# Kernel optimization log

Hardware: AMD Instinct MI355X
Metric: run time of the kernel (lower is better)

Reference implementation:

```python
import jax, jax.numpy as jnp
import numpy as np

N_NODES = 50000
N_EDGES = 600000
IN_DIM = 128
LATENT = 128
OUT_DIM = 40
NUM_LAYERS = 2


def setup_inputs() -> dict:
    key = jax.random.key(0)
    ks = jax.random.split(key, 8)
    nodes_feats = jax.random.normal(ks[0], (N_NODES, IN_DIM), dtype=jnp.float32)
    adj_list = jax.random.randint(ks[1], (N_EDGES, 2), 0, N_NODES, dtype=jnp.int64)
    s_in = 1.0 / np.sqrt(IN_DIM)
    s_cb = 1.0 / np.sqrt(2 * LATENT)
    s_out = 1.0 / np.sqrt(LATENT)
    W_in = jax.random.uniform(ks[2], (IN_DIM, LATENT), jnp.float32, -s_in, s_in)
    b_in = jnp.zeros((LATENT,), jnp.float32)
    W_comb = jax.random.uniform(ks[3], (NUM_LAYERS, 2 * LATENT, LATENT), jnp.float32, -s_cb, s_cb)
    b_comb = jnp.zeros((NUM_LAYERS, LATENT), jnp.float32)
    W_out = jax.random.uniform(ks[4], (LATENT, OUT_DIM), jnp.float32, -s_out, s_out)
    b_out = jnp.zeros((OUT_DIM,), jnp.float32)
    return {"nodes_feats": nodes_feats, "adj_list": adj_list, "W_in": W_in, "b_in": b_in,
            "W_comb": W_comb, "b_comb": b_comb, "W_out": W_out, "b_out": b_out}


def reference(nodes_feats, adj_list, W_in, b_in, W_comb, b_comb, W_out, b_out):
    n = nodes_feats.shape[0]
    fro = adj_list[:, 0]
    to = adj_list[:, 1]
    # initialize: project input features to latent space
    h = jax.nn.relu(nodes_feats @ W_in + b_in)  # [N, LATENT]
    # in-degree for mean aggregation (replaces per-node Python stack+mean)
    deg = jax.ops.segment_sum(jnp.ones(fro.shape[0], h.dtype), to, num_segments=n)
    inv_deg = 1.0 / jnp.maximum(deg, 1.0)  # guard isolated nodes
    for l in range(W_comb.shape[0]):
        # gather neighbor feats along edges, scatter-add to destinations, mean
        msg = jax.ops.segment_sum(h[fro], to, num_segments=n) * inv_deg[:, None]
        # combine: ReLU(Linear([node || message]))
        h = jax.nn.relu(jnp.concatenate([h, msg], axis=-1) @ W_comb[l] + b_comb[l])
    # output head (logits for CrossEntropyLoss)
    return h @ W_out + b_out
```

## Files before the change

kernel.cpp:

```cpp
#include <hip/hip_runtime.h>
#include <hip/hip_fp16.h>

#define N_NODES 50000
#define N_EDGES 600000
#define NBLK 49

typedef unsigned int u32;
typedef _Float16 v8h __attribute__((ext_vector_type(8)));
typedef _Float16 v4h __attribute__((ext_vector_type(4)));
typedef float v4f __attribute__((ext_vector_type(4)));

__device__ __forceinline__ float2 h2f2(u32 u) {
    __half2 h = *(__half2*)&u;
    return __half22float2(h);
}

__device__ __forceinline__ int calc_mode(const int* __restrict__ adj_w) {
    int l = threadIdx.x & 63;
    unsigned long long b = __ballot(adj_w[2 * l + 1] != 0);
    return (b == 0ull) ? 1 : 0;
}
__device__ __forceinline__ int adj_to(const int* a, int m, int e) {
    return m ? a[4 * e + 2] : a[2 * e + 1];
}
__device__ __forceinline__ int adj_fro(const int* a, int m, int e) {
    return m ? a[4 * e] : a[2 * e];
}

#define CNT_B   293
#define WPREP_B 344
#define IN_B    1563

__global__ void k_count_prep(const int* __restrict__ adj_w, int* __restrict__ deg,
                             int* __restrict__ rank,
                             const float* __restrict__ W_in,
                             const float* __restrict__ W_comb,
                             const float* __restrict__ W_out,
                             _Float16* __restrict__ WinT,
                             _Float16* __restrict__ WcombT,
                             _Float16* __restrict__ WoutT) {
    if (blockIdx.x < CNT_B) {
        int m = calc_mode(adj_w);
        int base = blockIdx.x * 2048 + threadIdx.x;
        int to[8], r[8];
#pragma unroll
        for (int i = 0; i < 8; i++) {
            int e = base + i * 256;
            to[i] = (e < N_EDGES) ? adj_to(adj_w, m, e) : -1;
        }
#pragma unroll
        for (int i = 0; i < 8; i++)
            if (to[i] >= 0) r[i] = atomicAdd(&deg[to[i]], 1);
#pragma unroll
        for (int i = 0; i < 8; i++) {
            int e = base + i * 256;
            if (e < N_EDGES) rank[e] = r[i];
        }
        return;
    }
    int idx = (blockIdx.x - CNT_B) * 256 + threadIdx.x;
    if (idx < 16384) {
        int n = idx & 127, k = idx >> 7;
        WinT[n * 128 + k] = (_Float16)W_in[k * 128 + n];
    } else if (idx < 16384 + 65536) {
        int j = idx - 16384;
        int l = j >> 15, r = j & 32767;
        int n = r & 127, k = r >> 7;
        WcombT[l * 32768 + n * 256 + k] = (_Float16)W_comb[l * 32768 + k * 128 + n];
    } else if (idx < 16384 + 65536 + 6144) {
        int j = idx - 81920;
        int n = j >> 7, k = j & 127;
        WoutT[n * 128 + k] = (n < 40) ? (_Float16)W_out[k * 40 + n] : (_Float16)0.f;
    }
}

__global__ void k_scan1(const int* __restrict__ deg, int* __restrict__ row_ptr,
                        int* __restrict__ bsum) {
    __shared__ int s[1024];
    int tid = threadIdx.x, i = blockIdx.x * 1024 + tid;
    int v = (i < N_NODES) ? deg[i] : 0;
    s[tid] = v;
    __syncthreads();
    for (int off = 1; off < 1024; off <<= 1) {
        int t = (tid >= off) ? s[tid - off] : 0;
        __syncthreads();
        s[tid] += t;
        __syncthreads();
    }
    if (i < N_NODES) row_ptr[i] = s[tid] - v;
    if (tid == 1023) bsum[blockIdx.x] = s[1023];
}

__global__ void k_scan23(const int* __restrict__ deg, int* __restrict__ row_ptr,
                         const int* __restrict__ bsum, float* __restrict__ inv_deg) {
    __shared__ int sbase;
    int tid = threadIdx.x;
    if (tid < 64) {
        int v = (tid < NBLK && tid < (int)blockIdx.x) ? bsum[tid] : 0;
#pragma unroll
        for (int off = 32; off > 0; off >>= 1) v += __shfl_down(v, off);
        if (tid == 0) sbase = v;
    }
    __syncthreads();
    int i = blockIdx.x * 1024 + tid;
    if (i < N_NODES) {
        row_ptr[i] = row_ptr[i] + sbase;
        inv_deg[i] = 1.0f / fmaxf((float)deg[i], 1.0f);
    }
    if (i == 0) row_ptr[N_NODES] = N_EDGES;
}

__global__ __launch_bounds__(256, 2) void k_fill_in(const int* __restrict__ adj_w,
                                                    const int* __restrict__ row_ptr,
                                                    const int* __restrict__ rank,
                                                    int* __restrict__ edge_src,
                                                    const float* __restrict__ X,
                                                    const _Float16* __restrict__ WT,
                                                    const float* __restrict__ bias,
                                                    _Float16* __restrict__ h) {
    __shared__ __align__(16) _Float16 xs[32][136];
    if (blockIdx.x < CNT_B) {
        int m = calc_mode(adj_w);
        int base = blockIdx.x * 2048 + threadIdx.x;
        int to[8], fro[8], rk[8];
#pragma unroll
        for (int i = 0; i < 8; i++) {
            int e = base + i * 256;
            if (e < N_EDGES) {
                to[i] = adj_to(adj_w, m, e);
                fro[i] = adj_fro(adj_w, m, e);
                rk[i] = rank[e];
            } else {
                to[i] = -1;
            }
        }
#pragma unroll
        for (int i = 0; i < 8; i++)
            if (to[i] >= 0) edge_src[row_ptr[to[i]] + rk[i]] = fro[i];
        return;
    }
    const int t0 = threadIdx.x, w = t0 >> 6, l = t0 & 63;
    const int R0 = (blockIdx.x - CNT_B) * 32;
    const float4* X4 = (const float4*)X;
#pragma unroll
    for (int i = 0; i < 4; i++) {
        int idx = i * 256 + t0;
        int row = idx >> 5, c4 = idx & 31;
        int rr = R0 + row;
        if (rr > N_NODES - 1) rr = N_NODES - 1;
        float4 v = X4[(size_t)rr * 32 + c4];
        v4h hv = {(_Float16)v.x, (_Float16)v.y, (_Float16)v.z, (_Float16)v.w};
        *(v4h*)&xs[row][c4 * 4] = hv;
    }
    const int ch = w & 1, rh = w >> 1;
    v8h wf[4][4];
#pragma unroll
    for (int t = 0; t < 4; t++)
#pragma unroll
        for (int s = 0; s < 4; s++) {
            int n = ch * 64 + t * 16 + (l & 15);
            int k = s * 32 + (l >> 4) * 8;
            wf[t][s] = *(const v8h*)&WT[n * 128 + k];
        }
    v4f acc[4];
#pragma unroll
    for (int t = 0; t < 4; t++) acc[t] = (v4f){0.f, 0.f, 0.f, 0.f};
    __syncthreads();
#pragma unroll
    for (int s = 0; s < 4; s++) {
        v8h a = *(const v8h*)&xs[rh * 16 + (l & 15)][s * 32 + (l >> 4) * 8];
#pragma unroll
        for (int t = 0; t < 4; t++)
            acc[t] = __builtin_amdgcn_mfma_f32_16x16x32_f16(a, wf[t][s], acc[t], 0, 0, 0);
    }
#pragma unroll
    for (int t = 0; t < 4; t++) {
        int col = ch * 64 + t * 16 + (l & 15);
        float b = bias[col];
#pragma unroll
        for (int i = 0; i < 4; i++) {
            int row = R0 + rh * 16 + (l >> 4) * 4 + i;
            if (row < N_NODES)
                h[(size_t)row * 128 + col] = (_Float16)fmaxf(acc[t][i] + b, 0.f);
        }
    }
}

__global__ __launch_bounds__(256) void k_gather(const uint2* __restrict__ h4,
                                                uint2* __restrict__ msg4,
                                                const int* __restrict__ row_ptr,
                                                const int* __restrict__ edge_src,
                                                const float* __restrict__ inv_deg) {
    const int w = threadIdx.x >> 6, l = threadIdx.x & 63;
    const int half = l >> 5, c = l & 31;
    const int wid = blockIdx.x * 4 + w, nw = gridDim.x * 4;
    for (int row = wid; row < N_NODES; row += nw) {
        const int e0 = row_ptr[row], e1 = row_ptr[row + 1];
        float a0 = 0.f, a1 = 0.f, a2 = 0.f, a3 = 0.f;
        for (int bse = e0; bse < e1; bse += 8) {
            uint2 v[4];
#pragma unroll
            for (int i = 0; i < 4; i++) {
                int ee = bse + 2 * i + half;
                int idx = (ee < e1) ? ee : (e1 - 1);
                v[i] = h4[(size_t)edge_src[idx] * 32 + c];
            }
#pragma unroll
            for (int i = 0; i < 4; i++) {
                if (bse + 2 * i + half < e1) {
                    float2 f0 = h2f2(v[i].x), f1 = h2f2(v[i].y);
                    a0 += f0.x;
                    a1 += f0.y;
                    a2 += f1.x;
                    a3 += f1.y;
                }
            }
        }
        a0 += __shfl_xor(a0, 32);
        a1 += __shfl_xor(a1, 32);
        a2 += __shfl_xor(a2, 32);
        a3 += __shfl_xor(a3, 32);
        if (half == 0) {
            const float inv = inv_deg[row];
            __half2 o0 = __floats2half2_rn(a0 * inv, a1 * inv);
            __half2 o1 = __floats2half2_rn(a2 * inv, a3 * inv);
            uint2 o;
            o.x = *(u32*)&o0;
            o.y = *(u32*)&o1;
            msg4[(size_t)row * 32 + c] = o;
        }
    }
}

__global__ __launch_bounds__(256, 2) void k_layer(const _Float16* __restrict__ hin,
                                                  const _Float16* __restrict__ msg,
                                                  const _Float16* __restrict__ WT,
                                                  const float* __restrict__ bias,
                                                  _Float16* __restrict__ hout) {
    __shared__ __align__(16) _Float16 xs[64][264];
    const int t0 = threadIdx.x, w = t0 >> 6, l = t0 & 63;
    const int R0 = blockIdx.x * 64;
    const uint4* h4 = (const uint4*)hin;
    const uint4* m4 = (const uint4*)msg;
#pragma unroll
    for (int i = 0; i < 8; i++) {
        int idx = i * 256 + t0;
        int row = idx >> 5, c16 = idx & 31;
        int rr = R0 + row;
        if (rr > N_NODES - 1) rr = N_NODES - 1;
        uint4 v = (c16 < 16) ? h4[(size_t)rr * 16 + c16] : m4[(size_t)rr * 16 + (c16 - 16)];
        *(uint4*)&xs[row][c16 * 8] = v;
    }
    const int ch = w & 1, rh = w >> 1;
    v8h wf[4][8];
#pragma unroll
    for (int t = 0; t < 4; t++)
#pragma unroll
        for (int s = 0; s < 8; s++) {
            int n = ch * 64 + t * 16 + (l & 15);
            int k = s * 32 + (l >> 4) * 8;
            wf[t][s] = *(const v8h*)&WT[n * 256 + k];
        }
    v4f acc[2][4];
#pragma unroll
    for (int sub = 0; sub < 2; sub++)
#pragma unroll
        for (int t = 0; t < 4; t++) acc[sub][t] = (v4f){0.f, 0.f, 0.f, 0.f};
    __syncthreads();
#pragma unroll
    for (int s = 0; s < 8; s++) {
#pragma unroll
        for (int sub = 0; sub < 2; sub++) {
            v8h a = *(const v8h*)&xs[rh * 32 + sub * 16 + (l & 15)][s * 32 + (l >> 4) * 8];
#pragma unroll
            for (int t = 0; t < 4; t++)
                acc[sub][t] = __builtin_amdgcn_mfma_f32_16x16x32_f16(a, wf[t][s], acc[sub][t], 0, 0, 0);
        }
    }
#pragma unroll
    for (int sub = 0; sub < 2; sub++)
#pragma unroll
        for (int t = 0; t < 4; t++) {
            int col = ch * 64 + t * 16 + (l & 15);
            float b = bias[col];
#pragma unroll
            for (int i = 0; i < 4; i++) {
                int row = R0 + rh * 32 + sub * 16 + (l >> 4) * 4 + i;
                if (row < N_NODES)
                    hout[(size_t)row * 128 + col] = (_Float16)fmaxf(acc[sub][t][i] + b, 0.f);
            }
        }
}

__global__ __launch_bounds__(256, 2) void k_layer_out(const _Float16* __restrict__ hin,
                                                      const _Float16* __restrict__ msg,
                                                      const _Float16* __restrict__ WT,
                                                      const float* __restrict__ bias,
                                                      const _Float16* __restrict__ WoT,
                                                      const float* __restrict__ bias_o,
                                                      float* __restrict__ outp) {
    __shared__ __align__(16) _Float16 xs[64][264];
    const int t0 = threadIdx.x, w = t0 >> 6, l = t0 & 63;
    const int R0 = blockIdx.x * 64;
    const uint4* h4 = (const uint4*)hin;
    const uint4* m4 = (const uint4*)msg;
#pragma unroll
    for (int i = 0; i < 8; i++) {
        int idx = i * 256 + t0;
        int row = idx >> 5, c16 = idx & 31;
        int rr = R0 + row;
        if (rr > N_NODES - 1) rr = N_NODES - 1;
        uint4 v = (c16 < 16) ? h4[(size_t)rr * 16 + c16] : m4[(size_t)rr * 16 + (c16 - 16)];
        *(uint4*)&xs[row][c16 * 8] = v;
    }
    const int ch = w & 1, rh = w >> 1;
    v8h wf[4][8];
#pragma unroll
    for (int t = 0; t < 4; t++)
#pragma unroll
        for (int s = 0; s < 8; s++) {
            int n = ch * 64 + t * 16 + (l & 15);
            int k = s * 32 + (l >> 4) * 8;
            wf[t][s] = *(const v8h*)&WT[n * 256 + k];
        }
    v4f acc[2][4];
#pragma unroll
    for (int sub = 0; sub < 2; sub++)
#pragma unroll
        for (int t = 0; t < 4; t++) acc[sub][t] = (v4f){0.f, 0.f, 0.f, 0.f};
    __syncthreads();
#pragma unroll
    for (int s = 0; s < 8; s++) {
#pragma unroll
        for (int sub = 0; sub < 2; sub++) {
            v8h a = *(const v8h*)&xs[rh * 32 + sub * 16 + (l & 15)][s * 32 + (l >> 4) * 8];
#pragma unroll
            for (int t = 0; t < 4; t++)
                acc[sub][t] = __builtin_amdgcn_mfma_f32_16x16x32_f16(a, wf[t][s], acc[sub][t], 0, 0, 0);
        }
    }
    __syncthreads();
    _Float16* hs = &xs[0][0];
#pragma unroll
    for (int sub = 0; sub < 2; sub++)
#pragma unroll
        for (int t = 0; t < 4; t++) {
            int col = ch * 64 + t * 16 + (l & 15);
            float b = bias[col];
#pragma unroll
            for (int i = 0; i < 4; i++) {
                int lrow = rh * 32 + sub * 16 + (l >> 4) * 4 + i;
                hs[lrow * 136 + col] = (_Float16)fmaxf(acc[sub][t][i] + b, 0.f);
            }
        }
    v8h wo[3][4];
#pragma unroll
    for (int t = 0; t < 3; t++)
#pragma unroll
        for (int s = 0; s < 4; s++) {
            int n = t * 16 + (l & 15);
            int k = s * 32 + (l >> 4) * 8;
            wo[t][s] = *(const v8h*)&WoT[n * 128 + k];
        }
    v4f acc2[3];
#pragma unroll
    for (int t = 0; t < 3; t++) acc2[t] = (v4f){0.f, 0.f, 0.f, 0.f};
    __syncthreads();
#pragma unroll
    for (int s = 0; s < 4; s++) {
        v8h a = *(const v8h*)&hs[(w * 16 + (l & 15)) * 136 + s * 32 + (l >> 4) * 8];
#pragma unroll
        for (int t = 0; t < 3; t++)
            acc2[t] = __builtin_amdgcn_mfma_f32_16x16x32_f16(a, wo[t][s], acc2[t], 0, 0, 0);
    }
#pragma unroll
    for (int t = 0; t < 3; t++) {
        int col = t * 16 + (l & 15);
        if (col < 40) {
            float b = bias_o[col];
#pragma unroll
            for (int i = 0; i < 4; i++) {
                int row = R0 + w * 16 + (l >> 4) * 4 + i;
                if (row < N_NODES) outp[(size_t)row * 40 + col] = acc2[t][i] + b;
            }
        }
    }
}

extern "C" void kernel_launch(void* const* d_in, const int* in_sizes, int n_in,
                              void* d_out, int out_size, void* d_ws, size_t ws_size,
                              hipStream_t stream) {
    int ix[8] = {0, 1, 2, 3, 4, 5, 6, 7};
    int tmp[8] = {-1, -1, -1, -1, -1, -1, -1, -1};
    for (int i = 0; i < n_in && i < 8; i++) {
        switch (in_sizes[i]) {
            case 6400000: tmp[0] = i; break;
            case 1200000: case 2400000: tmp[1] = i; break;
            case 16384:   tmp[2] = i; break;
            case 128:     tmp[3] = i; break;
            case 65536:   tmp[4] = i; break;
            case 256:     tmp[5] = i; break;
            case 5120:    tmp[6] = i; break;
            case 40:      tmp[7] = i; break;
        }
    }
    int found = 0;
    for (int j = 0; j < 8; j++) found += (tmp[j] >= 0);
    if (found == 8) for (int j = 0; j < 8; j++) ix[j] = tmp[j];

    const float* X      = (const float*)d_in[ix[0]];
    const int*   adj_w  = (const int*)d_in[ix[1]];
    const float* W_in   = (const float*)d_in[ix[2]];
    const float* b_in   = (const float*)d_in[ix[3]];
    const float* W_comb = (const float*)d_in[ix[4]];
    const float* b_comb = (const float*)d_in[ix[5]];
    const float* W_out  = (const float*)d_in[ix[6]];
    const float* b_out  = (const float*)d_in[ix[7]];
    float* out = (float*)d_out;

    char* base = (char*)d_ws;
    int*      deg      = (int*)(base + 0);
    int*      row_ptr  = (int*)(base + 200000);
    int*      rank     = (int*)(base + 400004);
    float*    inv_deg  = (float*)(base + 2800004);
    int*      edge_src = (int*)(base + 3000008);
    _Float16* WinT     = (_Float16*)(base + 5400016);
    _Float16* WcombT   = (_Float16*)(base + 5432784);
    _Float16* WoutT    = (_Float16*)(base + 5563856);
    _Float16* hA       = (_Float16*)(base + 5576144);
    _Float16* hB       = (_Float16*)(base + 18376144);
    _Float16* msg      = (_Float16*)(base + 31176144);
    int*      bsum     = (int*)hA;

    hipMemsetAsync(deg, 0, N_NODES * sizeof(int), stream);
    k_count_prep<<<CNT_B + WPREP_B, 256, 0, stream>>>(adj_w, deg, rank, W_in, W_comb, W_out,
                                                      WinT, WcombT, WoutT);
    k_scan1<<<NBLK, 1024, 0, stream>>>(deg, row_ptr, bsum);
    k_scan23<<<NBLK, 1024, 0, stream>>>(deg, row_ptr, bsum, inv_deg);
    k_fill_in<<<CNT_B + IN_B, 256, 0, stream>>>(adj_w, row_ptr, rank, edge_src,
                                                X, WinT, b_in, hA);

    k_gather<<<2048, 256, 0, stream>>>((const uint2*)hA, (uint2*)msg, row_ptr, edge_src, inv_deg);
    k_layer<<<782, 256, 0, stream>>>(hA, msg, WcombT, b_comb, hB);

    k_gather<<<2048, 256, 0, stream>>>((const uint2*)hB, (uint2*)msg, row_ptr, edge_src, inv_deg);
    k_layer_out<<<782, 256, 0, stream>>>(hB, msg, WcombT + 32768, b_comb + 128,
                                         WoutT, b_out, out);
}
```

Measured before the change: 254.8 us.

## Widen gather loads, fuse scan kernels via decoupled lookback, vectorize edge loads

The gather kernel now uses 16-byte loads, with four 16-lane groups each handling one edge and one row's 128 halves. It also prefetches the next row's row_ptr bounds. The two scan kernels are merged into one that passes block sums through flag-tagged atomics in the workspace, which removes one launch and the row_ptr re-read. Edge-list reads become single vector loads of (fro,to), and the memset now also clears the sync flags. The single-pass scan assumes all 49 blocks are co-resident, which holds on this GPU but adds spin-wait risk.

```diff
diff --git a/kernel.cpp b/kernel.cpp
--- a/kernel.cpp
+++ b/kernel.cpp
@@ -20,11 +20,17 @@
     unsigned long long b = __ballot(adj_w[2 * l + 1] != 0);
     return (b == 0ull) ? 1 : 0;
 }
-__device__ __forceinline__ int adj_to(const int* a, int m, int e) {
-    return m ? a[4 * e + 2] : a[2 * e + 1];
-}
-__device__ __forceinline__ int adj_fro(const int* a, int m, int e) {
-    return m ? a[4 * e] : a[2 * e];
+__device__ __forceinline__ void load_edge(const int* __restrict__ a, int m, int e,
+                                          int& fro, int& to) {
+    if (m) {
+        uint4 v = ((const uint4*)a)[e];
+        fro = (int)v.x;
+        to = (int)v.z;
+    } else {
+        uint2 v = ((const uint2*)a)[e];
+        fro = (int)v.x;
+        to = (int)v.y;
+    }
 }
 
 #define CNT_B   293
@@ -46,7 +52,12 @@
 #pragma unroll
         for (int i = 0; i < 8; i++) {
             int e = base + i * 256;
-            to[i] = (e < N_EDGES) ? adj_to(adj_w, m, e) : -1;
+            if (e < N_EDGES) {
+                int f;
+                load_edge(adj_w, m, e, f, to[i]);
+            } else {
+                to[i] = -1;
+            }
         }
 #pragma unroll
         for (int i = 0; i < 8; i++)
@@ -74,10 +85,12 @@
     }
 }
 
-__global__ void k_scan1(const int* __restrict__ deg, int* __restrict__ row_ptr,
-                        int* __restrict__ bsum) {
+__global__ void k_scan(const int* __restrict__ deg, int* __restrict__ row_ptr,
+                       float* __restrict__ inv_deg, int* __restrict__ bsync) {
     __shared__ int s[1024];
-    int tid = threadIdx.x, i = blockIdx.x * 1024 + tid;
+    __shared__ int sbase;
+    const int tid = threadIdx.x, b = blockIdx.x;
+    const int i = b * 1024 + tid;
     int v = (i < N_NODES) ? deg[i] : 0;
     s[tid] = v;
     __syncthreads();
@@ -87,25 +100,27 @@
         s[tid] += t;
         __syncthreads();
     }
-    if (i < N_NODES) row_ptr[i] = s[tid] - v;
-    if (tid == 1023) bsum[blockIdx.x] = s[1023];
-}
-
-__global__ void k_scan23(const int* __restrict__ deg, int* __restrict__ row_ptr,
-                         const int* __restrict__ bsum, float* __restrict__ inv_deg) {
-    __shared__ int sbase;
-    int tid = threadIdx.x;
+    if (tid == 1023)
+        __hip_atomic_store(&bsync[b], 0x40000000 | s[1023], __ATOMIC_RELEASE,
+                           __HIP_MEMORY_SCOPE_AGENT);
     if (tid < 64) {
-        int v = (tid < NBLK && tid < (int)blockIdx.x) ? bsum[tid] : 0;
-#pragma unroll
-        for (int off = 32; off > 0; off >>= 1) v += __shfl_down(v, off);
-        if (tid == 0) sbase = v;
-    }
-    __syncthreads();
-    int i = blockIdx.x * 1024 + tid;
+        int acc = 0;
+        if (tid < b) {
+            int x;
+            do {
+                x = __hip_atomic_load(&bsync[tid], __ATOMIC_ACQUIRE,
+                                      __HIP_MEMORY_SCOPE_AGENT);
+            } while (x < 0x40000000);
+            acc = x & 0x3fffffff;
+        }
+#pragma unroll
+        for (int off = 32; off > 0; off >>= 1) acc += __shfl_down(acc, off);
+        if (tid == 0) sbase = acc;
+    }
+    __syncthreads();
     if (i < N_NODES) {
-        row_ptr[i] = row_ptr[i] + sbase;
-        inv_deg[i] = 1.0f / fmaxf((float)deg[i], 1.0f);
+        row_ptr[i] = sbase + s[tid] - v;
+        inv_deg[i] = 1.0f / fmaxf((float)v, 1.0f);
     }
     if (i == 0) row_ptr[N_NODES] = N_EDGES;
 }
@@ -127,8 +142,7 @@
         for (int i = 0; i < 8; i++) {
             int e = base + i * 256;
             if (e < N_EDGES) {
-                to[i] = adj_to(adj_w, m, e);
-                fro[i] = adj_fro(adj_w, m, e);
+                load_edge(adj_w, m, e, fro[i], to[i]);
                 rk[i] = rank[e];
             } else {
                 to[i] = -1;
@@ -186,48 +200,66 @@
     }
 }
 
-__global__ __launch_bounds__(256) void k_gather(const uint2* __restrict__ h4,
-                                                uint2* __restrict__ msg4,
+__global__ __launch_bounds__(256) void k_gather(const uint4* __restrict__ h16,
+                                                uint4* __restrict__ msg16,
                                                 const int* __restrict__ row_ptr,
                                                 const int* __restrict__ edge_src,
                                                 const float* __restrict__ inv_deg) {
     const int w = threadIdx.x >> 6, l = threadIdx.x & 63;
-    const int half = l >> 5, c = l & 31;
+    const int grp = l >> 4, c = l & 15;
     const int wid = blockIdx.x * 4 + w, nw = gridDim.x * 4;
+    if (wid >= N_NODES) return;
+    int pe0 = row_ptr[wid], pe1 = row_ptr[wid + 1];
     for (int row = wid; row < N_NODES; row += nw) {
-        const int e0 = row_ptr[row], e1 = row_ptr[row + 1];
-        float a0 = 0.f, a1 = 0.f, a2 = 0.f, a3 = 0.f;
-        for (int bse = e0; bse < e1; bse += 8) {
-            uint2 v[4];
+        const int e0 = pe0, e1 = pe1;
+        const float inv = inv_deg[row];
+        const int nrow = row + nw;
+        if (nrow < N_NODES) {
+            pe0 = row_ptr[nrow];
+            pe1 = row_ptr[nrow + 1];
+        }
+        float a[8];
+#pragma unroll
+        for (int k = 0; k < 8; k++) a[k] = 0.f;
+        for (int bse = e0; bse < e1; bse += 16) {
+            uint4 v[4];
+            int ok[4];
 #pragma unroll
             for (int i = 0; i < 4; i++) {
-                int ee = bse + 2 * i + half;
-                int idx = (ee < e1) ? ee : (e1 - 1);
-                v[i] = h4[(size_t)edge_src[idx] * 32 + c];
+                int ee = bse + 4 * i + grp;
+                ok[i] = (ee < e1);
+                int idx = ok[i] ? ee : (e1 - 1);
+                v[i] = h16[(size_t)edge_src[idx] * 16 + c];
             }
 #pragma unroll
             for (int i = 0; i < 4; i++) {
-                if (bse + 2 * i + half < e1) {
-                    float2 f0 = h2f2(v[i].x), f1 = h2f2(v[i].y);
-                    a0 += f0.x;
-                    a1 += f0.y;
-                    a2 += f1.x;
-                    a3 += f1.y;
+                if (ok[i]) {
+                    u32 u[4] = {v[i].x, v[i].y, v[i].z, v[i].w};
+#pragma unroll
+                    for (int k = 0; k < 4; k++) {
+                        float2 f = h2f2(u[k]);
+                        a[2 * k] += f.x;
+                        a[2 * k + 1] += f.y;
+                    }
                 }
             }
         }
-        a0 += __shfl_xor(a0, 32);
-        a1 += __shfl_xor(a1, 32);
-        a2 += __shfl_xor(a2, 32);
-        a3 += __shfl_xor(a3, 32);
-        if (half == 0) {
-            const float inv = inv_deg[row];
-            __half2 o0 = __floats2half2_rn(a0 * inv, a1 * inv);
-            __half2 o1 = __floats2half2_rn(a2 * inv, a3 * inv);
-            uint2 o;
+#pragma unroll
+        for (int k = 0; k < 8; k++) {
+            a[k] += __shfl_xor(a[k], 16);
+            a[k] += __shfl_xor(a[k], 32);
+        }
+        if (grp == 0) {
+            __half2 o0 = __floats2half2_rn(a[0] * inv, a[1] * inv);
+            __half2 o1 = __floats2half2_rn(a[2] * inv, a[3] * inv);
+            __half2 o2 = __floats2half2_rn(a[4] * inv, a[5] * inv);
+            __half2 o3 = __floats2half2_rn(a[6] * inv, a[7] * inv);
+            uint4 o;
             o.x = *(u32*)&o0;
             o.y = *(u32*)&o1;
-            msg4[(size_t)row * 32 + c] = o;
+            o.z = *(u32*)&o2;
+            o.w = *(u32*)&o3;
+            msg16[(size_t)row * 16 + c] = o;
         }
     }
 }
@@ -420,30 +452,29 @@
 
     char* base = (char*)d_ws;
     int*      deg      = (int*)(base + 0);
-    int*      row_ptr  = (int*)(base + 200000);
-    int*      rank     = (int*)(base + 400004);
-    float*    inv_deg  = (float*)(base + 2800004);
-    int*      edge_src = (int*)(base + 3000008);
-    _Float16* WinT     = (_Float16*)(base + 5400016);
-    _Float16* WcombT   = (_Float16*)(base + 5432784);
-    _Float16* WoutT    = (_Float16*)(base + 5563856);
-    _Float16* hA       = (_Float16*)(base + 5576144);
-    _Float16* hB       = (_Float16*)(base + 18376144);
-    _Float16* msg      = (_Float16*)(base + 31176144);
-    int*      bsum     = (int*)hA;
-
-    hipMemsetAsync(deg, 0, N_NODES * sizeof(int), stream);
+    int*      bsync    = (int*)(base + 200000);
+    int*      row_ptr  = (int*)(base + 200256);
+    int*      rank     = (int*)(base + 400272);
+    float*    inv_deg  = (float*)(base + 2800272);
+    int*      edge_src = (int*)(base + 3000272);
+    _Float16* WinT     = (_Float16*)(base + 5400272);
+    _Float16* WcombT   = (_Float16*)(base + 5433040);
+    _Float16* WoutT    = (_Float16*)(base + 5564112);
+    _Float16* hA       = (_Float16*)(base + 5576448);
+    _Float16* hB       = (_Float16*)(base + 18376448);
+    _Float16* msg      = (_Float16*)(base + 31176448);
+
+    hipMemsetAsync(deg, 0, 200256, stream);
     k_count_prep<<<CNT_B + WPREP_B, 256, 0, stream>>>(adj_w, deg, rank, W_in, W_comb, W_out,
                                                       WinT, WcombT, WoutT);
-    k_scan1<<<NBLK, 1024, 0, stream>>>(deg, row_ptr, bsum);
-    k_scan23<<<NBLK, 1024, 0, stream>>>(deg, row_ptr, bsum, inv_deg);
+    k_scan<<<NBLK, 1024, 0, stream>>>(deg, row_ptr, inv_deg, bsync);
     k_fill_in<<<CNT_B + IN_B, 256, 0, stream>>>(adj_w, row_ptr, rank, edge_src,
                                                 X, WinT, b_in, hA);
 
-    k_gather<<<2048, 256, 0, stream>>>((const uint2*)hA, (uint2*)msg, row_ptr, edge_src, inv_deg);
+    k_gather<<<2048, 256, 0, stream>>>((const uint4*)hA, (uint4*)msg, row_ptr, edge_src, inv_deg);
     k_layer<<<782, 256, 0, stream>>>(hA, msg, WcombT, b_comb, hB);
 
-    k_gather<<<2048, 256, 0, stream>>>((const uint2*)hB, (uint2*)msg, row_ptr, edge_src, inv_deg);
+    k_gather<<<2048, 256, 0, stream>>>((const uint4*)hB, (uint4*)msg, row_ptr, edge_src, inv_deg);
     k_layer_out<<<782, 256, 0, stream>>>(hB, msg, WcombT + 32768, b_comb + 128,
                                          WoutT, b_out, out);
 }
```

Result: faster. 242.5 us, median of 2 (-4.9%).
